# Optimization experiments

Measured on AMD Instinct MI355X. Metric: run time of the kernel, lower is better.

## Reference

```python
import jax, jax.numpy as jnp
import numpy as np
from jax import lax

K = 3          # kernel size
STRIDE = 1
PAD = 1
DIL = 1


def conv2d(x, w, b, stride, pad):
    y = lax.conv_general_dilated(
        x, w, (stride, stride), [(pad, pad), (pad, pad)],
        dimension_numbers=('NCHW', 'OIHW', 'NCHW'))
    return y + b[None, :, None, None]


def deform_conv2d(x, offset, mask, weight, bias):
    # x: [B,C,H,W]; offset: [B,2*K*K,Ho,Wo] (channel 2i = y_i, 2i+1 = x_i);
    # mask: [B,K*K,Ho,Wo]; weight: [Cout,C,K,K]  (deformable_groups=1, groups=1)
    B, C, H, W = x.shape
    Ho, Wo = offset.shape[2], offset.shape[3]
    KK = K * K
    off = offset.reshape(B, KK, 2, Ho, Wo)
    off_y, off_x = off[:, :, 0], off[:, :, 1]          # [B,KK,Ho,Wo]

    ky, kx = jnp.meshgrid(jnp.arange(K), jnp.arange(K), indexing='ij')
    ky, kx = ky.ravel(), kx.ravel()                    # [KK]
    base_y = (jnp.arange(Ho) * STRIDE - PAD)[None, :, None] + (ky * DIL)[:, None, None]
    base_x = (jnp.arange(Wo) * STRIDE - PAD)[None, None, :] + (kx * DIL)[:, None, None]
    py = base_y[None].astype(x.dtype) + off_y          # [B,KK,Ho,Wo]
    px = base_x[None].astype(x.dtype) + off_x

    y0 = jnp.floor(py)
    x0 = jnp.floor(px)
    ly = py - y0
    lx = px - x0
    y0i = y0.astype(jnp.int32)
    x0i = x0.astype(jnp.int32)
    y1i = y0i + 1
    x1i = x0i + 1

    x_flat = x.reshape(B, C, H * W)

    def gather(yi, xi):
        valid = (yi >= 0) & (yi < H) & (xi >= 0) & (xi < W)
        idx = jnp.clip(yi, 0, H - 1) * W + jnp.clip(xi, 0, W - 1)
        v = jax.vmap(lambda xb, ib: xb[:, ib])(x_flat, idx.reshape(B, -1))
        v = v.reshape(B, C, KK, Ho, Wo)
        return v * valid[:, None].astype(x.dtype)

    w00 = ((1 - ly) * (1 - lx))[:, None]
    w01 = ((1 - ly) * lx)[:, None]
    w10 = (ly * (1 - lx))[:, None]
    w11 = (ly * lx)[:, None]
    samp = (w00 * gather(y0i, x0i) + w01 * gather(y0i, x1i)
            + w10 * gather(y1i, x0i) + w11 * gather(y1i, x1i))  # [B,C,KK,Ho,Wo]

    mod = samp * mask[:, None]                          # modulated samples
    wr = weight.reshape(weight.shape[0], C, KK)
    out = jnp.einsum('ocp,bcphw->bohw', wr, mod)
    return out + bias[None, :, None, None]


def setup_inputs() -> dict:
    key = jax.random.key(0)
    k1, k2, k3, k4, k5 = jax.random.split(key, 5)
    B, Cin, Cout, H, W = 4, 64, 128, 128, 128
    x = jax.random.normal(k1, (B, Cin, H, W), dtype=jnp.float32)
    # offset/mask conv: 3*K*K channels (o1, o2, mask). Zero-init in the source;
    # small random values here so nonzero offsets exercise the gather.
    offset_w = jax.random.normal(k2, (3 * K * K, Cin, K, K), dtype=jnp.float32) * 0.01
    offset_b = jax.random.normal(k3, (3 * K * K,), dtype=jnp.float32) * 0.01
    weight = jax.random.normal(k4, (Cout, Cin, K, K), dtype=jnp.float32) * (1.0 / np.sqrt(Cin * K * K))
    bias = jax.random.normal(k5, (Cout,), dtype=jnp.float32) * 0.01
    return {'x': x, 'offset_w': offset_w, 'offset_b': offset_b, 'weight': weight, 'bias': bias}


def reference(x, offset_w, offset_b, weight, bias):
    out = conv2d(x, offset_w, offset_b, STRIDE, PAD)    # [B,3*KK,Ho,Wo]
    o1, o2, m = jnp.split(out, 3, axis=1)
    offset = jnp.concatenate([o1, o2], axis=1)          # [B,2*KK,Ho,Wo]
    mask = jax.nn.sigmoid(m)                            # [B,KK,Ho,Wo]
    return deform_conv2d(x, offset, mask, weight, bias)
```

## Files before the change

### kernel.cpp

```cpp
#include <hip/hip_runtime.h>
#include <hip/hip_fp16.h>
#include <math.h>

#define HH   128
#define WW   128
#define HWP  16384
#define CIN  64
#define COUT 128

typedef float  f32x4  __attribute__((ext_vector_type(4)));
typedef short  short8 __attribute__((ext_vector_type(8)));

#define WBF_B    ((size_t)0)
#define OWBF_B   ((size_t)147456)
#define XT_B     ((size_t)221184)
#define META_B   ((size_t)8609792)
#define WS_NEED  ((size_t)8609792)
#define WS_NEED3 ((size_t)12148736)

__device__ inline unsigned short f2bf(float f) {
    unsigned u = __builtin_bit_cast(unsigned, f);
    return (unsigned short)((u + 0x7FFFu + ((u >> 16) & 1u)) >> 16);
}

__global__ __launch_bounds__(256) void k_prep(const float* __restrict__ x,
                                              const float* __restrict__ wgt,
                                              const float* __restrict__ ow,
                                              unsigned short* __restrict__ xt,
                                              unsigned short* __restrict__ wbf,
                                              unsigned short* __restrict__ owbf) {
    int t = threadIdx.x;
    if (blockIdx.x < 2048) {
        int bid  = blockIdx.x;
        int bid2 = (bid & 7) * 256 + (bid >> 3);
        int cgrp = t & 7, px = t >> 3;
        int pix = bid2 * 32 + px;
        int b = pix >> 14, hw = pix & 16383;
        const float* xp = x + (size_t)b * CIN * HWP + (size_t)(cgrp * 8) * HWP + hw;
        unsigned pk[4];
#pragma unroll
        for (int d = 0; d < 4; ++d) {
            float lo = xp[(size_t)(2 * d) * HWP];
            float hi = xp[(size_t)(2 * d + 1) * HWP];
            pk[d] = (unsigned)f2bf(lo) | ((unsigned)f2bf(hi) << 16);
        }
        *(uint4*)(xt + (size_t)pix * 64 + cgrp * 8) = *(uint4*)pk;
    } else {
        int tid = (blockIdx.x - 2048) * 256 + t;
        {
            int oc = tid / 576;
            int r  = tid - oc * 576;
            int kk = r >> 6;
            int c  = r & 63;
            wbf[tid] = f2bf(wgt[((size_t)oc * CIN + c) * 9 + kk]);
        }
        if (tid < 32 * 576) {
            int oc  = tid / 576;
            int r   = tid - oc * 576;
            int tap = r >> 6;
            int c   = r & 63;
            owbf[tid] = (oc < 27) ? f2bf(ow[((size_t)oc * CIN + c) * 9 + tap]) : 0;
        }
    }
}

__global__ __launch_bounds__(256) void k_offc(const unsigned short* __restrict__ xt,
                                              const unsigned short* __restrict__ owbf,
                                              const float* __restrict__ ob,
                                              __half* __restrict__ meta_h) {
    int blk0 = blockIdx.x;
    int blk  = (blk0 & 7) * 128 + (blk0 >> 3);
    int b    = blk >> 8;
    int rem  = blk & 255;
    int h    = (rem >> 2) * 2;
    int w0   = (rem & 3) << 5;
    int t    = threadIdx.x;
    int l    = t & 63;
    int wid  = t >> 6;
    int lm   = l & 15, lk = l >> 4;

    int r   = wid >> 1;
    int pxf = wid & 1;
    h += r;
    int spx = pxf * 16 + lm;

    const unsigned short* xbt = xt + (size_t)b * HWP * 64;
    f32x4 acc0 = {0.f,0.f,0.f,0.f};
    f32x4 acc1 = {0.f,0.f,0.f,0.f};
    const unsigned short* sab0 = owbf + (size_t)lm * 576 + lk * 8;
    const unsigned short* sab1 = sab0 + 16 * 576;

#pragma unroll
    for (int tap = 0; tap < 9; ++tap) {
        int ky = tap / 3, kx = tap % 3;
        int yy = h - 1 + ky;
        int xx = w0 - 1 + kx + spx;
        bool vld = (yy >= 0) && (yy < HH) && (xx >= 0) && (xx < WW);
        int yc = min(max(yy, 0), HH - 1), xc = min(max(xx, 0), WW - 1);
        const unsigned short* bp = xbt + (size_t)(yc * WW + xc) * 64 + lk * 8;
        uint4 v0 = *(const uint4*)bp;
        uint4 v1 = *(const uint4*)(bp + 32);
        if (!vld) { v0 = uint4{0,0,0,0}; v1 = uint4{0,0,0,0}; }
        short8 b0 = __builtin_bit_cast(short8, v0);
        short8 b1 = __builtin_bit_cast(short8, v1);
        short8 a00 = *(const short8*)(sab0 + tap * 64);
        short8 a01 = *(const short8*)(sab0 + tap * 64 + 32);
        short8 a10 = *(const short8*)(sab1 + tap * 64);
        short8 a11 = *(const short8*)(sab1 + tap * 64 + 32);
        acc0 = __builtin_amdgcn_mfma_f32_16x16x32_bf16(a00, b0, acc0, 0, 0, 0);
        acc0 = __builtin_amdgcn_mfma_f32_16x16x32_bf16(a01, b1, acc0, 0, 0, 0);
        acc1 = __builtin_amdgcn_mfma_f32_16x16x32_bf16(a10, b0, acc1, 0, 0, 0);
        acc1 = __builtin_amdgcn_mfma_f32_16x16x32_bf16(a11, b1, acc1, 0, 0, 0);
    }

    int hw = h * WW + w0 + spx;
#pragma unroll
    for (int q = 0; q < 4; ++q) {
        int oc0 = lk * 4 + q;
        float v0 = acc0[q] + ob[oc0];
        meta_h[((size_t)((oc0 & 1) * 9 + (oc0 >> 1)) * 4 + b) * HWP + hw] = __float2half(v0);
        int oc1 = 16 + lk * 4 + q;
        if (oc1 < 27) {
            float v1 = acc1[q] + ob[oc1];
            int comp, kk;
            if (oc1 < 18) { comp = oc1 & 1; kk = oc1 >> 1; }
            else          { comp = 2; kk = oc1 - 18; v1 = 1.f / (1.f + expf(-v1)); }
            meta_h[((size_t)(comp * 9 + kk) * 4 + b) * HWP + hw] = __float2half(v1);
        }
    }
}

__global__ __launch_bounds__(256) void k_main(const unsigned short* __restrict__ xt,
                                              const unsigned short* __restrict__ wbf,
                                              const __half* __restrict__ meta_h,
                                              const float* __restrict__ bias,
                                              float* __restrict__ out) {
    __shared__ __align__(16) char smem[11648];
    char*  mbase  = smem;
    float* meta_s = (float*)(smem + 8192);

    int blk0 = blockIdx.x;
    int blk  = (blk0 & 7) * 256 + (blk0 >> 3);
    int b   = blk >> 9;
    int rem = blk & 511;
    int h   = rem >> 2;
    int w0  = (rem & 3) << 5;
    int t   = threadIdx.x;

    int p1 = t >> 3;
    int cg = t & 7;
    int l  = t & 63;
    int wid = t >> 6;
    int lm = l & 15, lk = l >> 4;

    const unsigned short* xbt = xt + (size_t)b * HWP * 64;

    {
        int base_hw = h * WW + w0;
        for (int j = t; j < 864; j += 256) {
            int px = j & 31;
            int ck = j >> 5;
            float v = __half2float(meta_h[((size_t)ck * 4 + b) * HWP + base_hw + px]);
            int comp = ck / 9, kk = ck - comp * 9;
            meta_s[comp * 288 + kk * 32 + px] = v;
        }
    }
    __syncthreads();

    f32x4 acc00 = {0.f,0.f,0.f,0.f};
    f32x4 acc01 = {0.f,0.f,0.f,0.f};
    f32x4 acc10 = {0.f,0.f,0.f,0.f};
    f32x4 acc11 = {0.f,0.f,0.f,0.f};

    const unsigned short* arow0 = wbf + (size_t)(wid * 32 + lm) * 576 + lk * 8;
    const unsigned short* arow1 = arow0 + 16 * 576;

    int pA = lm, pB = lm + 16;
    int rbA = pA * 128, rbB = pB * 128;
    int swA = pA & 7,   swB = pB & 7;

    uint4 cc00, cc01, cc10, cc11;
    float cw00, cw01, cw10, cw11;

    const unsigned short* xbc = xbt + cg * 8;

#define PREF_CORNERS(KK) do {                                                  \
      int ky_ = (KK) / 3, kx_ = (KK) % 3;                                      \
      float offy = meta_s[(KK) * 32 + p1];                                     \
      float offx = meta_s[288 + (KK) * 32 + p1];                               \
      float msk  = meta_s[576 + (KK) * 32 + p1];                               \
      float py = (float)(h - 1 + ky_) + offy;                                  \
      float px = (float)(w0 + p1 - 1 + kx_) + offx;                            \
      float y0f = floorf(py), x0f = floorf(px);                                \
      float ly = py - y0f, lx = px - x0f;                                      \
      int y0 = (int)y0f, x0i = (int)x0f;                                       \
      int y1 = y0 + 1, x1 = x0i + 1;                                           \
      bool vy0 = (y0 >= 0) && (y0 < HH);                                       \
      bool vy1 = (y1 >= 0) && (y1 < HH);                                       \
      bool vx0 = (x0i >= 0) && (x0i < WW);                                     \
      bool vx1 = (x1 >= 0) && (x1 < WW);                                       \
      int yc0 = min(max(y0, 0), HH - 1), yc1 = min(max(y1, 0), HH - 1);        \
      int xc0 = min(max(x0i, 0), WW - 1), xc1 = min(max(x1, 0), WW - 1);       \
      cw00 = (1.f - ly) * (1.f - lx) * ((vy0 && vx0) ? msk : 0.f);             \
      cw01 = (1.f - ly) * lx         * ((vy0 && vx1) ? msk : 0.f);             \
      cw10 = ly * (1.f - lx)         * ((vy1 && vx0) ? msk : 0.f);             \
      cw11 = ly * lx                 * ((vy1 && vx1) ? msk : 0.f);             \
      cc00 = *(const uint4*)(xbc + (size_t)(yc0 * WW + xc0) * 64);             \
      cc01 = *(const uint4*)(xbc + (size_t)(yc0 * WW + xc1) * 64);             \
      cc10 = *(const uint4*)(xbc + (size_t)(yc1 * WW + xc0) * 64);             \
      cc11 = *(const uint4*)(xbc + (size_t)(yc1 * WW + xc1) * 64);             \
    } while (0)

    PREF_CORNERS(0);

#pragma unroll
    for (int kk = 0; kk < 9; ++kk) {
        const int cur = kk & 1;
        {
            char* wdst = mbase + cur * 4096;
            unsigned pk[4];
#pragma unroll
            for (int d = 0; d < 4; ++d) {
                unsigned u0 = (&cc00.x)[d], u1 = (&cc01.x)[d];
                unsigned u2 = (&cc10.x)[d], u3 = (&cc11.x)[d];
                float lo = cw00 * __builtin_bit_cast(float, u0 << 16)
                         + cw01 * __builtin_bit_cast(float, u1 << 16)
                         + cw10 * __builtin_bit_cast(float, u2 << 16)
                         + cw11 * __builtin_bit_cast(float, u3 << 16);
                float hi = cw00 * __builtin_bit_cast(float, u0 & 0xFFFF0000u)
                         + cw01 * __builtin_bit_cast(float, u1 & 0xFFFF0000u)
                         + cw10 * __builtin_bit_cast(float, u2 & 0xFFFF0000u)
                         + cw11 * __builtin_bit_cast(float, u3 & 0xFFFF0000u);
                pk[d] = (unsigned)f2bf(lo) | ((unsigned)f2bf(hi) << 16);
            }
            *(uint4*)(wdst + p1 * 128 + (((unsigned)(cg ^ (p1 & 7))) << 4)) = *(uint4*)pk;
        }
        if (kk < 8) PREF_CORNERS(kk + 1);
        asm volatile("s_waitcnt lgkmcnt(0)" ::: "memory");
        __builtin_amdgcn_s_barrier();
        __builtin_amdgcn_sched_barrier(0);
        const char* rb = mbase + cur * 4096;
#pragma unroll
        for (int sstep = 0; sstep < 2; ++sstep) {
            short8 a0 = *(const short8*)(arow0 + kk * 64 + sstep * 32);
            short8 a1 = *(const short8*)(arow1 + kk * 64 + sstep * 32);
            int kb = sstep * 4 + lk;
            short8 b0 = *(const short8*)(rb + rbA + ((kb ^ swA) << 4));
            short8 b1 = *(const short8*)(rb + rbB + ((kb ^ swB) << 4));
            acc00 = __builtin_amdgcn_mfma_f32_16x16x32_bf16(a0, b0, acc00, 0, 0, 0);
            acc01 = __builtin_amdgcn_mfma_f32_16x16x32_bf16(a0, b1, acc01, 0, 0, 0);
            acc10 = __builtin_amdgcn_mfma_f32_16x16x32_bf16(a1, b0, acc10, 0, 0, 0);
            acc11 = __builtin_amdgcn_mfma_f32_16x16x32_bf16(a1, b1, acc11, 0, 0, 0);
        }
    }
#undef PREF_CORNERS

    size_t outb = (size_t)b * COUT * HWP + (size_t)h * WW + w0;
#pragma unroll
    for (int of = 0; of < 2; ++of) {
        f32x4 aP = of ? acc10 : acc00;
        f32x4 aQ = of ? acc11 : acc01;
        int ocb = wid * 32 + of * 16 + lk * 4;
#pragma unroll
        for (int q = 0; q < 4; ++q) {
            int oc = ocb + q;
            float bi = bias[oc];
            out[outb + (size_t)oc * HWP + pA] = aP[q] + bi;
            out[outb + (size_t)oc * HWP + pB] = aQ[q] + bi;
        }
    }
}

__global__ __launch_bounds__(256) void k_fused_v2(const unsigned short* __restrict__ xt,
                                                  const unsigned short* __restrict__ wbf,
                                                  const unsigned short* __restrict__ owbf,
                                                  const float* __restrict__ ob,
                                                  const float* __restrict__ bias,
                                                  float* __restrict__ out) {
    __shared__ __align__(16) char smem[11648];
    char*  mbase  = smem;
    float* meta_s = (float*)(smem + 8192);

    int blk0 = blockIdx.x;
    int blk  = (blk0 & 7) * 256 + (blk0 >> 3);
    int b   = blk >> 9;
    int rem = blk & 511;
    int h   = rem >> 2;
    int w0  = (rem & 3) << 5;
    int t   = threadIdx.x;

    int p1 = t >> 3;
    int cg = t & 7;
    int l  = t & 63;
    int wid = t >> 6;
    int lm = l & 15, lk = l >> 4;

    const unsigned short* xbt = xt + (size_t)b * HWP * 64;

    int ocf = wid >> 1, pxf = wid & 1;
    int spx = pxf * 16 + lm;
    f32x4 sacc = {0.f, 0.f, 0.f, 0.f};
    const unsigned short* sab = owbf + (size_t)(ocf * 16 + lm) * 576 + lk * 8;

#pragma unroll
    for (int tap = 0; tap < 9; ++tap) {
        int ky = tap / 3, kx = tap % 3;
        int yy = h - 1 + ky;
        int xx = w0 - 1 + kx + spx;
        bool vld = (yy >= 0) && (yy < HH) && (xx >= 0) && (xx < WW);
        int yc = min(max(yy, 0), HH - 1), xc = min(max(xx, 0), WW - 1);
        const unsigned short* bp = xbt + (size_t)(yc * WW + xc) * 64 + lk * 8;
#pragma unroll
        for (int ch = 0; ch < 2; ++ch) {
            short8 a = *(const short8*)(sab + tap * 64 + ch * 32);
            uint4 v = *(const uint4*)(bp + ch * 32);
            v.x = vld ? v.x : 0u;  v.y = vld ? v.y : 0u;
            v.z = vld ? v.z : 0u;  v.w = vld ? v.w : 0u;
            sacc = __builtin_amdgcn_mfma_f32_16x16x32_bf16(a, __builtin_bit_cast(short8, v), sacc, 0, 0, 0);
        }
    }
#pragma unroll
    for (int q = 0; q < 4; ++q) {
        int oc = ocf * 16 + lk * 4 + q;
        if (oc < 27) {
            float v = sacc[q] + ob[oc];
            if (oc < 18) {
                meta_s[(oc & 1) * 288 + (oc >> 1) * 32 + spx] = v;
            } else {
                meta_s[2 * 288 + (oc - 18) * 32 + spx] = 1.f / (1.f + expf(-v));
            }
        }
    }
    __syncthreads();

    f32x4 acc00 = {0.f,0.f,0.f,0.f};
    f32x4 acc01 = {0.f,0.f,0.f,0.f};
    f32x4 acc10 = {0.f,0.f,0.f,0.f};
    f32x4 acc11 = {0.f,0.f,0.f,0.f};

    const unsigned short* arow0 = wbf + (size_t)(wid * 32 + lm) * 576 + lk * 8;
    const unsigned short* arow1 = arow0 + 16 * 576;

    int pA = lm, pB = lm + 16;
    int rbA = pA * 128, rbB = pB * 128;
    int swA = pA & 7,   swB = pB & 7;

    uint4 cc00, cc01, cc10, cc11;
    float cw00, cw01, cw10, cw11;

    const unsigned short* xbc = xbt + cg * 8;

#define PREF_CORNERS(KK) do {                                                  \
      int ky_ = (KK) / 3, kx_ = (KK) % 3;                                      \
      float offy = meta_s[(KK) * 32 + p1];                                     \
      float offx = meta_s[288 + (KK) * 32 + p1];                               \
      float msk  = meta_s[576 + (KK) * 32 + p1];                               \
      float py = (float)(h - 1 + ky_) + offy;                                  \
      float px = (float)(w0 + p1 - 1 + kx_) + offx;                            \
      float y0f = floorf(py), x0f = floorf(px);                                \
      float ly = py - y0f, lx = px - x0f;                                      \
      int y0 = (int)y0f, x0i = (int)x0f;                                       \
      int y1 = y0 + 1, x1 = x0i + 1;                                           \
      bool vy0 = (y0 >= 0) && (y0 < HH);                                       \
      bool vy1 = (y1 >= 0) && (y1 < HH);                                       \
      bool vx0 = (x0i >= 0) && (x0i < WW);                                     \
      bool vx1 = (x1 >= 0) && (x1 < WW);                                       \
      int yc0 = min(max(y0, 0), HH - 1), yc1 = min(max(y1, 0), HH - 1);        \
      int xc0 = min(max(x0i, 0), WW - 1), xc1 = min(max(x1, 0), WW - 1);       \
      cw00 = (1.f - ly) * (1.f - lx) * ((vy0 && vx0) ? msk : 0.f);             \
      cw01 = (1.f - ly) * lx         * ((vy0 && vx1) ? msk : 0.f);             \
      cw10 = ly * (1.f - lx)         * ((vy1 && vx0) ? msk : 0.f);             \
      cw11 = ly * lx                 * ((vy1 && vx1) ? msk : 0.f);             \
      cc00 = *(const uint4*)(xbc + (size_t)(yc0 * WW + xc0) * 64);             \
      cc01 = *(const uint4*)(xbc + (size_t)(yc0 * WW + xc1) * 64);             \
      cc10 = *(const uint4*)(xbc + (size_t)(yc1 * WW + xc0) * 64);             \
      cc11 = *(const uint4*)(xbc + (size_t)(yc1 * WW + xc1) * 64);             \
    } while (0)

    PREF_CORNERS(0);

#pragma unroll
    for (int kk = 0; kk < 9; ++kk) {
        const int cur = kk & 1;
        {
            char* wdst = mbase + cur * 4096;
            unsigned pk[4];
#pragma unroll
            for (int d = 0; d < 4; ++d) {
                unsigned u0 = (&cc00.x)[d], u1 = (&cc01.x)[d];
                unsigned u2 = (&cc10.x)[d], u3 = (&cc11.x)[d];
                float lo = cw00 * __builtin_bit_cast(float, u0 << 16)
                         + cw01 * __builtin_bit_cast(float, u1 << 16)
                         + cw10 * __builtin_bit_cast(float, u2 << 16)
                         + cw11 * __builtin_bit_cast(float, u3 << 16);
                float hi = cw00 * __builtin_bit_cast(float, u0 & 0xFFFF0000u)
                         + cw01 * __builtin_bit_cast(float, u1 & 0xFFFF0000u)
                         + cw10 * __builtin_bit_cast(float, u2 & 0xFFFF0000u)
                         + cw11 * __builtin_bit_cast(float, u3 & 0xFFFF0000u);
                pk[d] = (unsigned)f2bf(lo) | ((unsigned)f2bf(hi) << 16);
            }
            *(uint4*)(wdst + p1 * 128 + (((unsigned)(cg ^ (p1 & 7))) << 4)) = *(uint4*)pk;
        }
        if (kk < 8) PREF_CORNERS(kk + 1);
        asm volatile("s_waitcnt lgkmcnt(0)" ::: "memory");
        __builtin_amdgcn_s_barrier();
        __builtin_amdgcn_sched_barrier(0);
        const char* rb = mbase + cur * 4096;
#pragma unroll
        for (int sstep = 0; sstep < 2; ++sstep) {
            short8 a0 = *(const short8*)(arow0 + kk * 64 + sstep * 32);
            short8 a1 = *(const short8*)(arow1 + kk * 64 + sstep * 32);
            int kb = sstep * 4 + lk;
            short8 b0 = *(const short8*)(rb + rbA + ((kb ^ swA) << 4));
            short8 b1 = *(const short8*)(rb + rbB + ((kb ^ swB) << 4));
            acc00 = __builtin_amdgcn_mfma_f32_16x16x32_bf16(a0, b0, acc00, 0, 0, 0);
            acc01 = __builtin_amdgcn_mfma_f32_16x16x32_bf16(a0, b1, acc01, 0, 0, 0);
            acc10 = __builtin_amdgcn_mfma_f32_16x16x32_bf16(a1, b0, acc10, 0, 0, 0);
            acc11 = __builtin_amdgcn_mfma_f32_16x16x32_bf16(a1, b1, acc11, 0, 0, 0);
        }
    }
#undef PREF_CORNERS

    size_t outb = (size_t)b * COUT * HWP + (size_t)h * WW + w0;
#pragma unroll
    for (int of = 0; of < 2; ++of) {
        f32x4 aP = of ? acc10 : acc00;
        f32x4 aQ = of ? acc11 : acc01;
        int ocb = wid * 32 + of * 16 + lk * 4;
#pragma unroll
        for (int q = 0; q < 4; ++q) {
            int oc = ocb + q;
            float bi = bias[oc];
            out[outb + (size_t)oc * HWP + pA] = aP[q] + bi;
            out[outb + (size_t)oc * HWP + pB] = aQ[q] + bi;
        }
    }
}

extern "C" void kernel_launch(void* const* d_in, const int* in_sizes, int n_in,
                              void* d_out, int out_size, void* d_ws, size_t ws_size,
                              hipStream_t stream) {
    const float* x    = (const float*)d_in[0];
    const float* ow   = (const float*)d_in[1];
    const float* ob   = (const float*)d_in[2];
    const float* wgt  = (const float*)d_in[3];
    const float* bias = (const float*)d_in[4];
    float* out = (float*)d_out;
    char* ws = (char*)d_ws;

    unsigned short* wbf  = (unsigned short*)(ws + WBF_B);
    unsigned short* owbf = (unsigned short*)(ws + OWBF_B);
    unsigned short* xt   = (unsigned short*)(ws + XT_B);
    __half*         mh   = (__half*)(ws + META_B);

    hipLaunchKernelGGL(k_prep, dim3(2336), dim3(256), 0, stream,
                       x, wgt, ow, xt, wbf, owbf);
    if (ws_size >= WS_NEED3) {
        hipLaunchKernelGGL(k_offc, dim3(1024), dim3(256), 0, stream,
                           xt, owbf, ob, mh);
        hipLaunchKernelGGL(k_main, dim3(2048), dim3(256), 0, stream,
                           xt, wbf, mh, bias, out);
    } else {
        hipLaunchKernelGGL(k_fused_v2, dim3(2048), dim3(256), 0, stream,
                           xt, wbf, owbf, ob, bias, out);
    }
}
```

Measured before the change: 86.12 us.

## Stage offset-conv input halo in swizzled LDS and split output channels across waves

The offset/mask convolution kernel now loads a 3-row by 34-pixel halo tile of bf16 input into shared memory, using an XOR swizzle to avoid bank conflicts. All nine taps then read it from LDS instead of issuing repeated global loads. Each block now covers one row of 32 pixels. The four waves are split between two output-channel groups and two pixel halves, and the grid doubles to 2048 blocks. This cuts redundant global traffic and the number of MFMAs per wave, at the cost of a shared-memory fill, a barrier, and more blocks.

```diff
diff --git a/kernel.cpp b/kernel.cpp
--- a/kernel.cpp
+++ b/kernel.cpp
@@ -68,64 +68,68 @@
                                               const unsigned short* __restrict__ owbf,
                                               const float* __restrict__ ob,
                                               __half* __restrict__ meta_h) {
+    __shared__ __align__(16) char ctx[13056];
+
     int blk0 = blockIdx.x;
-    int blk  = (blk0 & 7) * 128 + (blk0 >> 3);
-    int b    = blk >> 8;
-    int rem  = blk & 255;
-    int h    = (rem >> 2) * 2;
-    int w0   = (rem & 3) << 5;
-    int t    = threadIdx.x;
-    int l    = t & 63;
-    int wid  = t >> 6;
-    int lm   = l & 15, lk = l >> 4;
-
-    int r   = wid >> 1;
-    int pxf = wid & 1;
-    h += r;
+    int blk  = (blk0 & 7) * 256 + (blk0 >> 3);
+    int b   = blk >> 9;
+    int rem = blk & 511;
+    int h   = rem >> 2;
+    int w0  = (rem & 3) << 5;
+    int t   = threadIdx.x;
+    int l   = t & 63;
+    int wid = t >> 6;
+    int lm  = l & 15, lk = l >> 4;
+
+    const unsigned short* xbt = xt + (size_t)b * HWP * 64;
+
+#pragma unroll
+    for (int c = 0; c < 4; ++c) {
+        int j = c * 256 + t;
+        if (j < 816) {
+            int g   = j / 34;
+            int px  = j - g * 34;
+            int row = g >> 3;
+            int cgj = g & 7;
+            int yy = h - 1 + row;
+            int xx = w0 - 1 + px;
+            bool vld = (yy >= 0) && (yy < HH) && (xx >= 0) && (xx < WW);
+            uint4 v = {0u, 0u, 0u, 0u};
+            if (vld) v = *(const uint4*)(xbt + (size_t)(yy * WW + xx) * 64 + cgj * 8);
+            *(uint4*)(ctx + (row * 34 + px) * 128 + ((cgj ^ (px & 7)) << 4)) = v;
+        }
+    }
+    __syncthreads();
+
+    int ocf = wid >> 1, pxf = wid & 1;
     int spx = pxf * 16 + lm;
-
-    const unsigned short* xbt = xt + (size_t)b * HWP * 64;
-    f32x4 acc0 = {0.f,0.f,0.f,0.f};
-    f32x4 acc1 = {0.f,0.f,0.f,0.f};
-    const unsigned short* sab0 = owbf + (size_t)lm * 576 + lk * 8;
-    const unsigned short* sab1 = sab0 + 16 * 576;
+    f32x4 sacc = {0.f, 0.f, 0.f, 0.f};
+    const unsigned short* sab = owbf + (size_t)(ocf * 16 + lm) * 576 + lk * 8;
 
 #pragma unroll
     for (int tap = 0; tap < 9; ++tap) {
         int ky = tap / 3, kx = tap % 3;
-        int yy = h - 1 + ky;
-        int xx = w0 - 1 + kx + spx;
-        bool vld = (yy >= 0) && (yy < HH) && (xx >= 0) && (xx < WW);
-        int yc = min(max(yy, 0), HH - 1), xc = min(max(xx, 0), WW - 1);
-        const unsigned short* bp = xbt + (size_t)(yc * WW + xc) * 64 + lk * 8;
-        uint4 v0 = *(const uint4*)bp;
-        uint4 v1 = *(const uint4*)(bp + 32);
-        if (!vld) { v0 = uint4{0,0,0,0}; v1 = uint4{0,0,0,0}; }
-        short8 b0 = __builtin_bit_cast(short8, v0);
-        short8 b1 = __builtin_bit_cast(short8, v1);
-        short8 a00 = *(const short8*)(sab0 + tap * 64);
-        short8 a01 = *(const short8*)(sab0 + tap * 64 + 32);
-        short8 a10 = *(const short8*)(sab1 + tap * 64);
-        short8 a11 = *(const short8*)(sab1 + tap * 64 + 32);
-        acc0 = __builtin_amdgcn_mfma_f32_16x16x32_bf16(a00, b0, acc0, 0, 0, 0);
-        acc0 = __builtin_amdgcn_mfma_f32_16x16x32_bf16(a01, b1, acc0, 0, 0, 0);
-        acc1 = __builtin_amdgcn_mfma_f32_16x16x32_bf16(a10, b0, acc1, 0, 0, 0);
-        acc1 = __builtin_amdgcn_mfma_f32_16x16x32_bf16(a11, b1, acc1, 0, 0, 0);
-    }
-
+        int cpx = kx + spx;
+        int crb = (ky * 34 + cpx) * 128;
+        int csw = cpx & 7;
+#pragma unroll
+        for (int ch = 0; ch < 2; ++ch) {
+            short8 a  = *(const short8*)(sab + tap * 64 + ch * 32);
+            int kb = ch * 4 + lk;
+            short8 bf = *(const short8*)(ctx + crb + (((unsigned)(kb ^ csw)) << 4));
+            sacc = __builtin_amdgcn_mfma_f32_16x16x32_bf16(a, bf, sacc, 0, 0, 0);
+        }
+    }
     int hw = h * WW + w0 + spx;
 #pragma unroll
     for (int q = 0; q < 4; ++q) {
-        int oc0 = lk * 4 + q;
-        float v0 = acc0[q] + ob[oc0];
-        meta_h[((size_t)((oc0 & 1) * 9 + (oc0 >> 1)) * 4 + b) * HWP + hw] = __float2half(v0);
-        int oc1 = 16 + lk * 4 + q;
-        if (oc1 < 27) {
-            float v1 = acc1[q] + ob[oc1];
+        int oc = ocf * 16 + lk * 4 + q;
+        if (oc < 27) {
+            float v = sacc[q] + ob[oc];
             int comp, kk;
-            if (oc1 < 18) { comp = oc1 & 1; kk = oc1 >> 1; }
-            else          { comp = 2; kk = oc1 - 18; v1 = 1.f / (1.f + expf(-v1)); }
-            meta_h[((size_t)(comp * 9 + kk) * 4 + b) * HWP + hw] = __float2half(v1);
+            if (oc < 18) { comp = oc & 1; kk = oc >> 1; }
+            else         { comp = 2; kk = oc - 18; v = 1.f / (1.f + expf(-v)); }
+            meta_h[((size_t)(comp * 9 + kk) * 4 + b) * HWP + hw] = __float2half(v);
         }
     }
 }
@@ -456,7 +460,7 @@
     hipLaunchKernelGGL(k_prep, dim3(2336), dim3(256), 0, stream,
                        x, wgt, ow, xt, wbf, owbf);
     if (ws_size >= WS_NEED3) {
-        hipLaunchKernelGGL(k_offc, dim3(1024), dim3(256), 0, stream,
+        hipLaunchKernelGGL(k_offc, dim3(2048), dim3(256), 0, stream,
                            xt, owbf, ob, mh);
         hipLaunchKernelGGL(k_main, dim3(2048), dim3(256), 0, stream,
                            xt, wbf, mh, bias, out);
```

Measured after the change: 80.66 us (median of 2 runs). 1.07x faster.
